# Kernel tuning notes

Hardware: AMD Instinct MI355X
Metric: run time of the kernel (lower is better)

## Reference

```python
import jax, jax.numpy as jnp
import numpy as np

B, T, WIN, HID = 256, 16384, 5, 5  # hidden must equal window for mse_loss shapes to match


def setup_inputs() -> dict:
    key = jax.random.key(0)
    k1, k2, k3 = jax.random.split(key, 3)
    series = jax.random.normal(k1, (B, T), dtype=jnp.float32)
    # nn.Linear(window_size, hidden_size) params: weight [H, W], bias [H]
    bound = 1.0 / np.sqrt(WIN)
    weight = jax.random.uniform(k2, (HID, WIN), jnp.float32, -bound, bound)
    bias = jax.random.uniform(k3, (HID,), jnp.float32, -bound, bound)
    threshold = jnp.float32(0.1)  # change_point_threshold parameter
    return {"series": series, "weight": weight, "bias": bias, "threshold": threshold}


def reference(series, weight, bias, threshold):
    Bb, Tt = series.shape
    H, Wd = weight.shape
    N = Tt - Wd  # number of windows = time_steps - window_size
    # Gather all sliding windows at once: idx [N, W]
    idx = jnp.arange(N)[:, None] + jnp.arange(Wd)[None, :]
    local = series[:, idx]        # [B, N, W]  == series[:, i:i+W] for all i
    target = series[:, idx + 1]   # [B, N, W]  == series[:, i+1:i+W+1]
    # Tiny per-window linear, batched over all windows
    transformed = jnp.einsum('bnw,hw->bnh', local, weight) + bias  # [B, N, H]
    # F.mse_loss reduces over all elements (B and H) per window
    losses = jnp.mean((transformed - target) ** 2, axis=(0, 2))    # [N]
    # change-point logic vectorized: diff of consecutive losses vs threshold
    diffs = jnp.abs(losses[1:] - losses[:-1])                      # [N-1]
    change_mask = diffs > threshold                                # [N-1] bool
    return losses, diffs, change_mask
```

## Files before the change

### kernel.cpp

```cpp
#include <hip/hip_runtime.h>

#define BB    256
#define TT    16384
#define WIN   5
#define HID   5
#define NN    (TT - WIN)
#define TILE  32
#define NT    512
#define LDSW  44

__global__ __launch_bounds__(256)
void llsa_fused(const float* __restrict__ series,
                const float* __restrict__ weight,
                const float* __restrict__ bias,
                const float* __restrict__ thr_ptr,
                float* __restrict__ out) {
    const int tid = threadIdx.x;
    const int t  = (blockIdx.x & 7) * 64 + (blockIdx.x >> 3);
    const int n0 = t * TILE;

    float w[HID][WIN], bi[HID];
#pragma unroll
    for (int h = 0; h < HID; ++h) {
        bi[h] = bias[h];
#pragma unroll
        for (int v = 0; v < WIN; ++v) w[h][v] = weight[h * WIN + v];
    }

    __shared__ float lds[BB * LDSW];
    __shared__ float psum[32 * 33];
    __shared__ float Ls[TILE + 1];

    {
        const int c4 = (tid & 7) * 4;
        const int rb = tid >> 3;
#pragma unroll
        for (int it = 0; it < 8; ++it) {
            const int r = it * 32 + rb;
            const float4 v = *(const float4*)(series + (size_t)r * TT + n0 + c4);
            *(float4*)(&lds[r * LDSW + c4]) = v;
        }
    }
    {
#pragma unroll
        for (int it = 0; it < 2; ++it) {
            const int idx = it * 256 + tid;
            const int r   = idx >> 1;
            const int cc  = 32 + (idx & 1) * 4;
            const int col = n0 + cc;
            float4 v = make_float4(0.f, 0.f, 0.f, 0.f);
            if (col + 3 < TT) {
                v = *(const float4*)(series + (size_t)r * TT + col);
            }
            *(float4*)(&lds[r * LDSW + cc]) = v;
        }
    }
    __syncthreads();

    const int cq = tid & 7;
    const int rs = tid >> 3;
    float a0 = 0.f, a1 = 0.f, a2 = 0.f, a3 = 0.f;
#pragma unroll
    for (int k = 0; k < 8; ++k) {
        const float* row = &lds[(rs * 8 + k) * LDSW + 4 * cq];
        const float4 f0 = *(const float4*)(row);
        const float4 f1 = *(const float4*)(row + 4);
        const float4 f2 = *(const float4*)(row + 8);
        const float s[12] = { f0.x, f0.y, f0.z, f0.w,
                              f1.x, f1.y, f1.z, f1.w,
                              f2.x, f2.y, f2.z, f2.w };
#pragma unroll
        for (int j = 0; j < 4; ++j) {
            float aj = 0.f;
#pragma unroll
            for (int h = 0; h < HID; ++h) {
                float tt = bi[h];
#pragma unroll
                for (int v = 0; v < WIN; ++v) tt = fmaf(s[j + v], w[h][v], tt);
                const float e = tt - s[j + h + 1];
                aj = fmaf(e, e, aj);
            }
            if (j == 0) a0 += aj; else if (j == 1) a1 += aj;
            else if (j == 2) a2 += aj; else a3 += aj;
        }
    }

    float bacc = 0.f;
    if (tid < 64) {
#pragma unroll
        for (int sIt = 0; sIt < 4; ++sIt) {
            const float* row = &lds[(tid + 64 * sIt) * LDSW + TILE];
            float sv[WIN + 1];
#pragma unroll
            for (int j = 0; j <= WIN; ++j) sv[j] = row[j];
#pragma unroll
            for (int h = 0; h < HID; ++h) {
                float tt = bi[h];
#pragma unroll
                for (int v = 0; v < WIN; ++v) tt = fmaf(sv[v], w[h][v], tt);
                const float e = tt - sv[h + 1];
                bacc = fmaf(e, e, bacc);
            }
        }
    }
    float bs = bacc;
#pragma unroll
    for (int off = 32; off >= 1; off >>= 1) bs += __shfl_down(bs, off);

    psum[rs * 33 + 4 * cq + 0] = a0;
    psum[rs * 33 + 4 * cq + 1] = a1;
    psum[rs * 33 + 4 * cq + 2] = a2;
    psum[rs * 33 + 4 * cq + 3] = a3;
    const float inv = 1.0f / (float)(BB * HID);
    if (tid == 0) Ls[TILE] = bs * inv;
    __syncthreads();

    if (tid < TILE) {
        float s = 0.f;
#pragma unroll
        for (int r = 0; r < 32; ++r) s += psum[r * 33 + tid];
        Ls[tid] = s * inv;
    }
    __syncthreads();

    if (tid < TILE) {
        const int i = n0 + tid;
        if (i < NN) {
            const float li = Ls[tid];
            out[i] = li;
            if (i < NN - 1) {
                const float d = fabsf(Ls[tid + 1] - li);
                out[NN + i] = d;
                out[2 * NN - 1 + i] = (d > thr_ptr[0]) ? 1.0f : 0.0f;
            }
        }
    }
}

extern "C" void kernel_launch(void* const* d_in, const int* in_sizes, int n_in,
                              void* d_out, int out_size, void* d_ws, size_t ws_size,
                              hipStream_t stream) {
    const float* series = (const float*)d_in[0];
    const float* weight = (const float*)d_in[1];
    const float* bias   = (const float*)d_in[2];
    const float* thr    = (const float*)d_in[3];
    float* out = (float*)d_out;
    (void)d_ws; (void)ws_size; (void)in_sizes; (void)n_in; (void)out_size;

    llsa_fused<<<NT, 256, 0, stream>>>(series, weight, bias, thr, out);
}
```

Measured before the change: 73.34 us.

## Stream batch rows through double-buffered LDS chunks with register prefetch

```diff
diff --git a/kernel.cpp b/kernel.cpp
--- a/kernel.cpp
+++ b/kernel.cpp
@@ -8,6 +8,8 @@
 #define TILE  32
 #define NT    512
 #define LDSW  44
+#define CH    64
+#define NCH   4
 
 __global__ __launch_bounds__(256)
 void llsa_fused(const float* __restrict__ series,
@@ -27,72 +29,69 @@
         for (int v = 0; v < WIN; ++v) w[h][v] = weight[h * WIN + v];
     }
 
-    __shared__ float lds[BB * LDSW];
+    __shared__ float lds[2][CH * LDSW];
     __shared__ float psum[32 * 33];
-    __shared__ float Ls[TILE + 1];
-
-    {
-        const int c4 = (tid & 7) * 4;
-        const int rb = tid >> 3;
-#pragma unroll
-        for (int it = 0; it < 8; ++it) {
-            const int r = it * 32 + rb;
-            const float4 v = *(const float4*)(series + (size_t)r * TT + n0 + c4);
-            *(float4*)(&lds[r * LDSW + c4]) = v;
-        }
-    }
-    {
-#pragma unroll
-        for (int it = 0; it < 2; ++it) {
-            const int idx = it * 256 + tid;
-            const int r   = idx >> 1;
-            const int cc  = 32 + (idx & 1) * 4;
-            const int col = n0 + cc;
-            float4 v = make_float4(0.f, 0.f, 0.f, 0.f);
-            if (col + 3 < TT) {
-                v = *(const float4*)(series + (size_t)r * TT + col);
-            }
-            *(float4*)(&lds[r * LDSW + cc]) = v;
-        }
-    }
-    __syncthreads();
 
     const int cq = tid & 7;
     const int rs = tid >> 3;
-    float a0 = 0.f, a1 = 0.f, a2 = 0.f, a3 = 0.f;
+
+    float4 ra0, ra1, rb;
+    const int bcol = n0 + 32 + (tid & 1) * 4;
+    const bool bok = (bcol + 3) < TT;
+
+    auto GLOAD = [&](int c) {
+        const int rbase = c * CH;
+        ra0 = *(const float4*)(series + (size_t)(rbase + rs)      * TT + n0 + 4*cq);
+        ra1 = *(const float4*)(series + (size_t)(rbase + 32 + rs) * TT + n0 + 4*cq);
+        if (tid < 128) {
+            rb = bok ? *(const float4*)(series + (size_t)(rbase + (tid >> 1)) * TT + bcol)
+                     : make_float4(0.f, 0.f, 0.f, 0.f);
+        }
+    };
+    auto SWRITE = [&](int b) {
+        *(float4*)(&lds[b][(rs)      * LDSW + 4*cq]) = ra0;
+        *(float4*)(&lds[b][(32 + rs) * LDSW + 4*cq]) = ra1;
+        if (tid < 128) *(float4*)(&lds[b][(tid >> 1) * LDSW + 32 + (tid & 1) * 4]) = rb;
+    };
+
+    GLOAD(0); SWRITE(0);
+    GLOAD(1);
+    __syncthreads();
+
+    float a0 = 0.f, a1 = 0.f, a2 = 0.f, a3 = 0.f, bacc = 0.f;
+
 #pragma unroll
-    for (int k = 0; k < 8; ++k) {
-        const float* row = &lds[(rs * 8 + k) * LDSW + 4 * cq];
-        const float4 f0 = *(const float4*)(row);
-        const float4 f1 = *(const float4*)(row + 4);
-        const float4 f2 = *(const float4*)(row + 8);
-        const float s[12] = { f0.x, f0.y, f0.z, f0.w,
-                              f1.x, f1.y, f1.z, f1.w,
-                              f2.x, f2.y, f2.z, f2.w };
+    for (int c = 0; c < NCH; ++c) {
+        const int cur = c & 1;
 #pragma unroll
-        for (int j = 0; j < 4; ++j) {
-            float aj = 0.f;
+        for (int it2 = 0; it2 < 2; ++it2) {
+            const float* row = &lds[cur][(it2 * 32 + rs) * LDSW + 4 * cq];
+            const float4 f0 = *(const float4*)(row);
+            const float4 f1 = *(const float4*)(row + 4);
+            const float4 f2 = *(const float4*)(row + 8);
+            const float s[12] = { f0.x, f0.y, f0.z, f0.w,
+                                  f1.x, f1.y, f1.z, f1.w,
+                                  f2.x, f2.y, f2.z, f2.w };
 #pragma unroll
-            for (int h = 0; h < HID; ++h) {
-                float tt = bi[h];
+            for (int j = 0; j < 4; ++j) {
+                float aj = 0.f;
 #pragma unroll
-                for (int v = 0; v < WIN; ++v) tt = fmaf(s[j + v], w[h][v], tt);
-                const float e = tt - s[j + h + 1];
-                aj = fmaf(e, e, aj);
+                for (int h = 0; h < HID; ++h) {
+                    float tt = bi[h];
+#pragma unroll
+                    for (int v = 0; v < WIN; ++v) tt = fmaf(s[j + v], w[h][v], tt);
+                    const float e = tt - s[j + h + 1];
+                    aj = fmaf(e, e, aj);
+                }
+                if (j == 0) a0 += aj; else if (j == 1) a1 += aj;
+                else if (j == 2) a2 += aj; else a3 += aj;
             }
-            if (j == 0) a0 += aj; else if (j == 1) a1 += aj;
-            else if (j == 2) a2 += aj; else a3 += aj;
         }
-    }
-
-    float bacc = 0.f;
-    if (tid < 64) {
-#pragma unroll
-        for (int sIt = 0; sIt < 4; ++sIt) {
-            const float* row = &lds[(tid + 64 * sIt) * LDSW + TILE];
-            float sv[WIN + 1];
-#pragma unroll
-            for (int j = 0; j <= WIN; ++j) sv[j] = row[j];
+        if (tid < 64) {
+            const float* r2 = &lds[cur][tid * LDSW + 32];
+            const float4 q0 = *(const float4*)(r2);
+            const float2 q1 = *(const float2*)(r2 + 4);
+            const float sv[6] = { q0.x, q0.y, q0.z, q0.w, q1.x, q1.y };
 #pragma unroll
             for (int h = 0; h < HID; ++h) {
                 float tt = bi[h];
@@ -102,34 +101,37 @@
                 bacc = fmaf(e, e, bacc);
             }
         }
+        if (c + 1 < NCH) {
+            SWRITE((c + 1) & 1);
+            if (c + 2 < NCH) GLOAD(c + 2);
+        }
+        __syncthreads();
     }
+
     float bs = bacc;
 #pragma unroll
     for (int off = 32; off >= 1; off >>= 1) bs += __shfl_down(bs, off);
+    const float bL = __shfl(bs, 0);
 
     psum[rs * 33 + 4 * cq + 0] = a0;
     psum[rs * 33 + 4 * cq + 1] = a1;
     psum[rs * 33 + 4 * cq + 2] = a2;
     psum[rs * 33 + 4 * cq + 3] = a3;
-    const float inv = 1.0f / (float)(BB * HID);
-    if (tid == 0) Ls[TILE] = bs * inv;
     __syncthreads();
 
-    if (tid < TILE) {
-        float s = 0.f;
+    if (tid < 32) {
+        const float inv = 1.0f / (float)(BB * HID);
+        float ssum = 0.f;
 #pragma unroll
-        for (int r = 0; r < 32; ++r) s += psum[r * 33 + tid];
-        Ls[tid] = s * inv;
-    }
-    __syncthreads();
-
-    if (tid < TILE) {
+        for (int r = 0; r < 32; ++r) ssum += psum[r * 33 + tid];
+        const float li = ssum * inv;
+        float nx = __shfl_down(li, 1);
+        if (tid == 31) nx = bL * inv;
         const int i = n0 + tid;
         if (i < NN) {
-            const float li = Ls[tid];
             out[i] = li;
             if (i < NN - 1) {
-                const float d = fabsf(Ls[tid + 1] - li);
+                const float d = fabsf(nx - li);
                 out[NN + i] = d;
                 out[2 * NN - 1 + i] = (d > thr_ptr[0]) ? 1.0f : 0.0f;
             }
```

After: 72.67 us. Within noise of the previous version (-0.9%).
